# Kernel optimization log

Measured on AMD Instinct MI355X. Metric: run time of the kernel, lower is better.

The kernel has to match this reference:

```python
import jax, jax.numpy as jnp
import numpy as np

B, C, D = 4, 1024, 1024
H, DH = 16, 64  # num_heads, head_size; D == H*DH


def setup_inputs() -> dict:
    key = jax.random.key(0)
    ks = jax.random.split(key, 8)
    return {
        "query_input": jax.random.normal(ks[0], (B, C, D), dtype=jnp.float32),
        "key_input": jax.random.normal(ks[1], (B, C, D), dtype=jnp.float32),
        "value_input": jax.random.normal(ks[2], (B, C, D), dtype=jnp.float32),
        "Wq": jax.random.normal(ks[3], (D, D), dtype=jnp.float32) * 0.02,
        "Wk": jax.random.normal(ks[4], (D, D), dtype=jnp.float32) * 0.02,
        "Wv": jax.random.normal(ks[5], (D, D), dtype=jnp.float32) * 0.02,
        "Wp": jax.random.normal(ks[6], (D, D), dtype=jnp.float32) * 0.02,
        "bp": jax.random.normal(ks[7], (D,), dtype=jnp.float32) * 0.02,
        "mask": jnp.zeros((C, C), dtype=bool),
    }


def _split_heads(x):
    # (B, C, D) -> (B, H, C, DH)
    return x.reshape(B, C, H, DH).transpose(0, 2, 1, 3)


def reference(query_input, key_input, value_input, Wq, Wk, Wv, Wp, bp, mask):
    scale = DH ** -0.5
    q = _split_heads(query_input @ Wq.T)
    k = _split_heads(key_input @ Wk.T)
    v = _split_heads(value_input @ Wv.T)
    # ||q_i - k_j||_2 via norm decomposition: |q|^2 + |k|^2 - 2 q.k
    q2 = jnp.sum(q * q, axis=-1)  # (B, H, C)
    k2 = jnp.sum(k * k, axis=-1)  # (B, H, C)
    qk = jnp.einsum("bhqd,bhkd->bhqk", q, k)  # (B, H, C, C)
    sq = jnp.maximum(q2[..., :, None] + k2[..., None, :] - 2.0 * qk, 0.0)
    wei = jnp.sqrt(sq) * scale
    wei = jnp.where(mask, -jnp.inf, wei)
    wei = jax.nn.softmax(wei, axis=-1)
    out = jnp.einsum("bhqk,bhkd->bhqd", wei, v)  # (B, H, C, DH)
    out = out.transpose(0, 2, 1, 3).reshape(B, C, D)
    return out @ Wp.T + bp
```

## Files before the change

### kernel.cpp

```cpp
#include <hip/hip_runtime.h>


typedef _Float16 f16;
typedef __attribute__((ext_vector_type(2))) _Float16 f16x2;
typedef __attribute__((ext_vector_type(8))) _Float16 f16x8;
typedef __attribute__((ext_vector_type(4))) float f32x4;
typedef __attribute__((ext_vector_type(16))) float f32x16;

#define MFMA16(a, b, c) __builtin_amdgcn_mfma_f32_16x16x32_f16((a), (b), (c), 0, 0, 0)
#define MFMA32(a, b, c) __builtin_amdgcn_mfma_f32_32x32x16_f16((a), (b), (c), 0, 0, 0)

constexpr double LOG2E = 1.4426950408889634;
constexpr double C2d = 0.015625 * LOG2E * LOG2E;

#if __has_builtin(__builtin_amdgcn_exp2f)
#define EXP2F(x) __builtin_amdgcn_exp2f(x)
#else
#define EXP2F(x) exp2f(x)
#endif
#if __has_builtin(__builtin_amdgcn_sqrtf)
#define SQRTF(x) __builtin_amdgcn_sqrtf(x)
#else
#define SQRTF(x) sqrtf(x)
#endif

__device__ __forceinline__ void stage16(const void* g, void* lds_base_uniform) {
#if __has_builtin(__builtin_amdgcn_global_load_lds)
    __builtin_amdgcn_global_load_lds((const __attribute__((address_space(1))) void*)g,
                                     (__attribute__((address_space(3))) void*)lds_base_uniform,
                                     16, 0, 0);
#else
    const int lane = threadIdx.x & 63;
    *(f16x8*)((f16*)lds_base_uniform + lane * 8) = *(const f16x8*)g;
#endif
}

__device__ __forceinline__ f16x8 cvt8v(f32x4 a, f32x4 b) {
    f16x8 o;
    o[0] = (f16)a[0]; o[1] = (f16)a[1]; o[2] = (f16)a[2]; o[3] = (f16)a[3];
    o[4] = (f16)b[0]; o[5] = (f16)b[1]; o[6] = (f16)b[2]; o[7] = (f16)b[3];
    return o;
}

__global__ __launch_bounds__(256) void cvt_all(const float* __restrict__ Xq,
                                               const float* __restrict__ Xk,
                                               const float* __restrict__ Xv,
                                               const float* __restrict__ Wq,
                                               const float* __restrict__ Wk,
                                               const float* __restrict__ Wv,
                                               const float* __restrict__ Wp,
                                               f16* __restrict__ W16,
                                               f16* __restrict__ X16) {
    const size_t idx = (size_t)blockIdx.x * 2048 + threadIdx.x * 8;
    const size_t M4 = 4ull << 20, M1 = 1ull << 20;
    const float* s;
    f16* d;
    if (idx < 3 * M4) {
        if (idx < M4) s = Xq + idx;
        else if (idx < 2 * M4) s = Xk + (idx - M4);
        else s = Xv + (idx - 2 * M4);
        d = X16 + idx;
    } else {
        size_t wi = idx - 3 * M4;
        if (wi < M1) s = Wq + wi;
        else if (wi < 2 * M1) s = Wk + (wi - M1);
        else if (wi < 3 * M1) s = Wv + (wi - 2 * M1);
        else s = Wp + (wi - 3 * M1);
        d = W16 + wi;
    }
    f32x4 a = *(const f32x4*)s;
    f32x4 b = *(const f32x4*)(s + 4);
    *(f16x8*)d = cvt8v(a, b);
}

template <int MODE>
__global__ __launch_bounds__(256, 2) void gemm(const f16* __restrict__ A,
                                               const f16* __restrict__ B,
                                               f16* __restrict__ Co,
                                               float* __restrict__ Cf,
                                               const float* __restrict__ bias,
                                               float* __restrict__ nrm,
                                               float osc0, float osc1,
                                               float ns0, float ns1,
                                               int M, int N, int K) {
    constexpr bool NORMS = (MODE == 0);
    constexpr bool F32OUT = (MODE == 2);
    __shared__ __attribute__((aligned(16))) f16 As[128 * 64];
    __shared__ __attribute__((aligned(16))) f16 Bs[128 * 64];
    const int tid = threadIdx.x;
    const int lane = tid & 63;
    const int w = tid >> 6;
    const int l31 = lane & 31, l5 = lane >> 5;
    const int z = blockIdx.z;
    const f16* Ap = (MODE == 0) ? A + (size_t)z * (4u << 20) : A;
    const f16* Bp = (MODE == 0) ? B + (size_t)z * (1u << 20) : B;
    f16* Cop = (MODE == 0) ? Co + (size_t)z * (4u << 20) : Co;
    float* nrmp = NORMS ? nrm + (size_t)z * 65536 : nullptr;
    const float osc = z ? osc1 : osc0;
    const float nscale = z ? ns1 : ns0;
    const int wr = (w >> 1) * 64, wc = (w & 1) * 64;
    const int nwg = gridDim.x * gridDim.y;
    const int f = blockIdx.y * gridDim.x + blockIdx.x;
    const int g = (f & 7) * (nwg >> 3) + (f >> 3);
    const int row0 = (g / gridDim.x) * 128;
    const int col0 = (g % gridDim.x) * 128;

    f32x16 acc[2][2] = {};

    for (int kt = 0; kt < K; kt += 64) {
        __syncthreads();
#pragma unroll
        for (int t = 0; t < 4; ++t) {
            const int rb = w * 32 + t * 8;
            const int rr = rb + (lane >> 3);
            const int gs = (lane & 7) ^ (rr & 7);
            stage16(&Ap[(size_t)(row0 + rr) * K + kt + gs * 8], &As[rb * 64]);
            stage16(&Bp[(size_t)(col0 + rr) * K + kt + gs * 8], &Bs[rb * 64]);
        }
        __syncthreads();
#pragma unroll
        for (int ks = 0; ks < 4; ++ks) {
            const int gq = ks * 2 + l5;
            f16x8 af[2], bf[2];
#pragma unroll
            for (int mr = 0; mr < 2; ++mr)
                af[mr] = *(const f16x8*)&As[(wr + mr * 32 + l31) * 64 + ((gq ^ (l31 & 7)) * 8)];
#pragma unroll
            for (int n2 = 0; n2 < 2; ++n2)
                bf[n2] = *(const f16x8*)&Bs[(wc + n2 * 32 + l31) * 64 + ((gq ^ (l31 & 7)) * 8)];
#pragma unroll
            for (int mr = 0; mr < 2; ++mr)
#pragma unroll
                for (int n2 = 0; n2 < 2; ++n2) acc[mr][n2] = MFMA32(af[mr], bf[n2], acc[mr][n2]);
        }
    }

    const int cc0 = col0 + wc + l31;
    const int cc1 = col0 + wc + 32 + l31;
    const int hh = (col0 + wc) >> 6;
#pragma unroll
    for (int mr = 0; mr < 2; ++mr)
#pragma unroll
        for (int j = 0; j < 16; ++j) {
            const int rr = row0 + wr + mr * 32 + (j & 3) + 8 * (j >> 2) + 4 * l5;
            if (F32OUT) {
                Cf[(size_t)rr * N + cc0] = acc[mr][0][j] + bias[cc0];
                Cf[(size_t)rr * N + cc1] = acc[mr][1][j] + bias[cc1];
            } else {
                const f16 h0 = (f16)(acc[mr][0][j] * osc);
                const f16 h1 = (f16)(acc[mr][1][j] * osc);
                if (NORMS) {
                    float v0 = (float)h0, v1 = (float)h1;
                    float s = v0 * v0 + v1 * v1;
                    s += __shfl_xor(s, 1);
                    s += __shfl_xor(s, 2);
                    s += __shfl_xor(s, 4);
                    s += __shfl_xor(s, 8);
                    s += __shfl_xor(s, 16);
                    if (l31 == 0)
                        nrmp[(size_t)((rr >> 10) * 16 + hh) * 1024 + (rr & 1023)] = s * nscale;
                }
                Cop[(size_t)rr * N + cc0] = h0;
                Cop[(size_t)rr * N + cc1] = h1;
            }
        }
}

__global__ __launch_bounds__(256, 2) void attn(const f16* __restrict__ qs,
                                               const f16* __restrict__ kb,
                                               const f16* __restrict__ vT,
                                               const float* __restrict__ q2c2,
                                               const float* __restrict__ k2c2,
                                               f16* __restrict__ out) {
    __shared__ __attribute__((aligned(16))) f16 Ks[128 * 64];
    __shared__ __attribute__((aligned(16))) f16 Vs[64 * 128];
    __shared__ float k2tile[128];
    const int tid = threadIdx.x;
    const int lane = tid & 63;
    const int w = tid >> 6;
    const int l15 = lane & 15, l4 = lane >> 4;
    const int fid = blockIdx.y * 8 + blockIdx.x;
    const int qt = (fid >> 3) & 7;
    const int bh = (fid & 7) * 8 + (fid >> 6);
    const int b = bh >> 4, h = bh & 15;
    const int wq = w * 32;
    const int hcol = h * 64;
    const int qrow0 = b * 1024 + qt * 128;
    const f16* vTh = vT + (size_t)hcol * 4096 + b * 1024;

    const int sr = tid >> 3, sc0 = (tid & 7) * 8;
    const int vr = tid >> 4, vc0 = (tid & 15) * 8;
    const int vsw = (vr & 7) << 3;
    const int fsw = (l15 & 7) << 3;

    f16x8 bq[2][2];
#pragma unroll
    for (int m = 0; m < 2; ++m)
#pragma unroll
        for (int ks = 0; ks < 2; ++ks)
            bq[m][ks] = *(const f16x8*)&qs[(size_t)(qrow0 + wq + m * 16 + l15) * 1024 + hcol + ks * 32 + l4 * 8];
    float q2m[2];
#pragma unroll
    for (int m = 0; m < 2; ++m) q2m[m] = q2c2[(size_t)bh * 1024 + qt * 128 + wq + m * 16 + l15];

    f32x4 accv[2][4] = {};
    f32x4 dacc[2] = {};
    const f16 one = (f16)1.f;
    const f16x8 ones8 = {one, one, one, one, one, one, one, one};

    f16x8 kreg[4], vreg[4];
    float k2reg = 0.f;
#define ISSUE_LOADS(KT)                                                                                      \
    {                                                                                                        \
        _Pragma("unroll") for (int i = 0; i < 4; ++i)                                                        \
            kreg[i] = *(const f16x8*)&kb[(size_t)(b * 1024 + (KT) * 128 + sr + i * 32) * 1024 + hcol + sc0]; \
        _Pragma("unroll") for (int j = 0; j < 4; ++j)                                                        \
            vreg[j] = *(const f16x8*)&vTh[(size_t)(vr + j * 16) * 4096 + (KT) * 128 + vc0];                  \
        k2reg = (tid < 128) ? k2c2[(size_t)bh * 1024 + (KT) * 128 + tid] : 0.f;                              \
    }

    ISSUE_LOADS(0)

    for (int kt = 0; kt < 8; ++kt) {
        __syncthreads();
#pragma unroll
        for (int i = 0; i < 4; ++i) {
            const int kap = sr + i * 32;
            const int s = ((kap >> 5) & 3) * 32 + ((kap >> 2) & 1) * 16 + ((kap >> 3) & 3) * 4 + (kap & 3);
            *(f16x8*)&Ks[s * 64 + (sc0 ^ ((s & 7) << 3))] = kreg[i];
        }
#pragma unroll
        for (int j = 0; j < 4; ++j) *(f16x8*)&Vs[(vr + j * 16) * 128 + (vc0 ^ vsw)] = vreg[j];
        if (tid < 128) k2tile[tid] = k2reg;
        __syncthreads();
        if (kt < 7) ISSUE_LOADS(kt + 1)

#pragma unroll
        for (int kk = 0; kk < 4; ++kk) {
            unsigned um[2][4];
#pragma unroll
            for (int half = 0; half < 2; ++half) {
                const int n = kk * 2 + half;
                f16x8 kf0 = *(const f16x8*)&Ks[(n * 16 + l15) * 64 + ((l4 * 8) ^ fsw)];
                f16x8 kf1 = *(const f16x8*)&Ks[(n * 16 + l15) * 64 + ((32 + l4 * 8) ^ fsw)];
                f32x4 k2q = *(const f32x4*)&k2tile[kk * 32 + l4 * 8 + half * 4];
#pragma unroll
                for (int m = 0; m < 2; ++m) {
                    f32x4 c0;
#pragma unroll
                    for (int r = 0; r < 4; ++r) c0[r] = q2m[m] + k2q[r];
                    f32x4 st = MFMA16(kf0, bq[m][0], c0);
                    st = MFMA16(kf1, bq[m][1], st);
                    float p0 = EXP2F(SQRTF(fmaxf(st[0], 0.f)));
                    float p1 = EXP2F(SQRTF(fmaxf(st[1], 0.f)));
                    float p2 = EXP2F(SQRTF(fmaxf(st[2], 0.f)));
                    float p3 = EXP2F(SQRTF(fmaxf(st[3], 0.f)));
                    f16x2 lo = {(f16)p0, (f16)p1};
                    f16x2 hi = {(f16)p2, (f16)p3};
                    um[m][half * 2] = __builtin_bit_cast(unsigned, lo);
                    um[m][half * 2 + 1] = __builtin_bit_cast(unsigned, hi);
                }
            }
            f16x8 ap[2];
#pragma unroll
            for (int m = 0; m < 2; ++m) {
                uint4 u = {um[m][0], um[m][1], um[m][2], um[m][3]};
                ap[m] = __builtin_bit_cast(f16x8, u);
            }
#pragma unroll
            for (int m = 0; m < 2; ++m) dacc[m] = MFMA16(ap[m], ones8, dacc[m]);
#pragma unroll
            for (int n2 = 0; n2 < 4; ++n2) {
                f16x8 bv = *(const f16x8*)&Vs[(n2 * 16 + l15) * 128 + ((kk * 32 + l4 * 8) ^ fsw)];
#pragma unroll
                for (int m = 0; m < 2; ++m) accv[m][n2] = MFMA16(ap[m], bv, accv[m][n2]);
            }
        }
    }

#pragma unroll
    for (int m = 0; m < 2; ++m)
#pragma unroll
        for (int r = 0; r < 4; ++r) {
            const float rd = 1.0f / dacc[m][r];
#pragma unroll
            for (int n2 = 0; n2 < 4; ++n2)
                out[(size_t)(qrow0 + wq + m * 16 + l4 * 4 + r) * 1024 + hcol + n2 * 16 + l15] =
                    (f16)(accv[m][n2][r] * rd);
        }
}

extern "C" void kernel_launch(void* const* d_in, const int* in_sizes, int n_in,
                              void* d_out, int out_size, void* d_ws, size_t ws_size,
                              hipStream_t stream) {
    const float* Xq = (const float*)d_in[0];
    const float* Xk = (const float*)d_in[1];
    const float* Xv = (const float*)d_in[2];
    const float* Wq = (const float*)d_in[3];
    const float* Wk = (const float*)d_in[4];
    const float* Wv = (const float*)d_in[5];
    const float* Wp = (const float*)d_in[6];
    const float* bp = (const float*)d_in[7];
    float* out = (float*)d_out;

    char* ws = (char*)d_ws;
    f16* W16 = (f16*)(ws);
    f16* X16 = (f16*)(ws + (8ull << 20));
    f16* vTb = (f16*)(ws + (8ull << 20));
    f16* attnout = (f16*)(ws + (16ull << 20));
    f16* Xv16 = (f16*)(ws + (24ull << 20));
    f16* qb = (f16*)(ws + (32ull << 20));
    f16* kb = (f16*)(ws + (40ull << 20));
    float* q2c2 = out;
    float* k2c2 = out + 65536;

    const float qsc = (float)(-2.0 * C2d);
    const float ns_q = (float)(1.0 / (4.0 * C2d));
    const float ns_k = (float)C2d;

    cvt_all<<<8192, 256, 0, stream>>>(Xq, Xk, Xv, Wq, Wk, Wv, Wp, W16, X16);

    gemm<0><<<dim3(8, 32, 2), 256, 0, stream>>>(
        X16, W16, qb, nullptr, nullptr, q2c2, qsc, 1.0f, ns_q, ns_k, 4096, 1024, 1024);

    gemm<1><<<dim3(32, 8), 256, 0, stream>>>(
        W16 + 2 * (1u << 20), Xv16, vTb, nullptr, nullptr, nullptr,
        1.0f, 1.0f, 0.f, 0.f, 1024, 4096, 1024);

    attn<<<dim3(8, 64), 256, 0, stream>>>(qb, kb, vTb, q2c2, k2c2, attnout);

    gemm<2><<<dim3(8, 32), 256, 0, stream>>>(
        attnout, W16 + 3 * (1u << 20), nullptr, out, bp, nullptr,
        1.0f, 1.0f, 0.f, 0.f, 4096, 1024, 1024);
}
```

Measured before the change: 119.3 us.

## Split attention KV loop across two thread groups and merge QKV gemm launches

The attention kernel now runs 512 threads per block. Two groups of 256 each process half of the key tiles, and their partial accumulators are reduced through shared memory before normalisation. The Q/K and V projection gemms are merged into one launch, and the output projection uses 64x128 tiles to double the block count. MFMA sections get raised wave priority. The aim is more parallelism and fewer launches, at the cost of higher LDS use per block and an extra reduction step.

```diff
diff --git a/kernel.cpp b/kernel.cpp
--- a/kernel.cpp
+++ b/kernel.cpp
@@ -73,37 +73,21 @@
     *(f16x8*)d = cvt8v(a, b);
 }
 
-template <int MODE>
-__global__ __launch_bounds__(256, 2) void gemm(const f16* __restrict__ A,
-                                               const f16* __restrict__ B,
-                                               f16* __restrict__ Co,
-                                               float* __restrict__ Cf,
-                                               const float* __restrict__ bias,
-                                               float* __restrict__ nrm,
-                                               float osc0, float osc1,
-                                               float ns0, float ns1,
-                                               int M, int N, int K) {
-    constexpr bool NORMS = (MODE == 0);
-    constexpr bool F32OUT = (MODE == 2);
-    __shared__ __attribute__((aligned(16))) f16 As[128 * 64];
-    __shared__ __attribute__((aligned(16))) f16 Bs[128 * 64];
+template <bool NORMS, bool F32OUT>
+__device__ __forceinline__ void gemm128(f16* As, f16* Bs,
+                                        const f16* __restrict__ Ap,
+                                        const f16* __restrict__ Bp,
+                                        f16* __restrict__ Cop,
+                                        float* __restrict__ Cf,
+                                        const float* __restrict__ bias,
+                                        float* __restrict__ nrmp,
+                                        float osc, float nscale,
+                                        int row0, int col0, int N, int K) {
     const int tid = threadIdx.x;
     const int lane = tid & 63;
     const int w = tid >> 6;
     const int l31 = lane & 31, l5 = lane >> 5;
-    const int z = blockIdx.z;
-    const f16* Ap = (MODE == 0) ? A + (size_t)z * (4u << 20) : A;
-    const f16* Bp = (MODE == 0) ? B + (size_t)z * (1u << 20) : B;
-    f16* Cop = (MODE == 0) ? Co + (size_t)z * (4u << 20) : Co;
-    float* nrmp = NORMS ? nrm + (size_t)z * 65536 : nullptr;
-    const float osc = z ? osc1 : osc0;
-    const float nscale = z ? ns1 : ns0;
     const int wr = (w >> 1) * 64, wc = (w & 1) * 64;
-    const int nwg = gridDim.x * gridDim.y;
-    const int f = blockIdx.y * gridDim.x + blockIdx.x;
-    const int g = (f & 7) * (nwg >> 3) + (f >> 3);
-    const int row0 = (g / gridDim.x) * 128;
-    const int col0 = (g % gridDim.x) * 128;
 
     f32x16 acc[2][2] = {};
 
@@ -166,30 +150,126 @@
         }
 }
 
-__global__ __launch_bounds__(256, 2) void attn(const f16* __restrict__ qs,
+__global__ __launch_bounds__(256, 2) void gemm_qkv(const f16* __restrict__ X16,
+                                                   const f16* __restrict__ W16,
+                                                   f16* __restrict__ qb_base,
+                                                   f16* __restrict__ vTb,
+                                                   float* __restrict__ nrm,
+                                                   float qsc, float ns_q, float ns_k) {
+    __shared__ __attribute__((aligned(16))) f16 As[128 * 64];
+    __shared__ __attribute__((aligned(16))) f16 Bs[128 * 64];
+    const int bid = blockIdx.x;
+    if (bid < 512) {
+        const int z = bid >> 8;
+        const int f = bid & 255;
+        const int g = (f & 7) * 32 + (f >> 3);
+        const int row0 = (g >> 3) * 128, col0 = (g & 7) * 128;
+        gemm128<true, false>(As, Bs,
+                             X16 + (size_t)z * (4u << 20), W16 + (size_t)z * (1u << 20),
+                             qb_base + (size_t)z * (4u << 20), nullptr, nullptr,
+                             nrm + (size_t)z * 65536,
+                             z ? 1.0f : qsc, z ? ns_k : ns_q, row0, col0, 1024, 1024);
+    } else {
+        const int f = bid - 512;
+        const int g = (f & 7) * 32 + (f >> 3);
+        const int row0 = (g >> 5) * 128, col0 = (g & 31) * 128;
+        gemm128<false, false>(As, Bs,
+                              W16 + 2 * (1u << 20), X16 + 2 * (4u << 20),
+                              vTb, nullptr, nullptr, nullptr,
+                              1.0f, 0.f, row0, col0, 4096, 1024);
+    }
+}
+
+__global__ __launch_bounds__(256, 2) void gemm_fin(const f16* __restrict__ A,
+                                                   const f16* __restrict__ B,
+                                                   float* __restrict__ Cf,
+                                                   const float* __restrict__ bias) {
+    __shared__ __attribute__((aligned(16))) f16 As[64 * 64];
+    __shared__ __attribute__((aligned(16))) f16 Bs[128 * 64];
+    const int tid = threadIdx.x;
+    const int lane = tid & 63;
+    const int w = tid >> 6;
+    const int l31 = lane & 31, l5 = lane >> 5;
+    const int wr = (w & 1) * 32, wc = (w >> 1) * 64;
+    const int f = blockIdx.x;
+    const int g = (f & 7) * 64 + (f >> 3);
+    const int row0 = (g >> 3) * 64, col0 = (g & 7) * 128;
+    const int K = 1024, N = 1024;
+
+    f32x16 acc[2] = {};
+
+    for (int kt = 0; kt < K; kt += 64) {
+        __syncthreads();
+#pragma unroll
+        for (int t = 0; t < 2; ++t) {
+            const int rb = w * 16 + t * 8;
+            const int rr = rb + (lane >> 3);
+            const int gs = (lane & 7) ^ (rr & 7);
+            stage16(&A[(size_t)(row0 + rr) * K + kt + gs * 8], &As[rb * 64]);
+        }
+#pragma unroll
+        for (int t = 0; t < 4; ++t) {
+            const int rb = w * 32 + t * 8;
+            const int rr = rb + (lane >> 3);
+            const int gs = (lane & 7) ^ (rr & 7);
+            stage16(&B[(size_t)(col0 + rr) * K + kt + gs * 8], &Bs[rb * 64]);
+        }
+        __syncthreads();
+#pragma unroll
+        for (int ks = 0; ks < 4; ++ks) {
+            const int gq = ks * 2 + l5;
+            f16x8 af = *(const f16x8*)&As[(wr + l31) * 64 + ((gq ^ (l31 & 7)) * 8)];
+#pragma unroll
+            for (int n2 = 0; n2 < 2; ++n2) {
+                f16x8 bf = *(const f16x8*)&Bs[(wc + n2 * 32 + l31) * 64 + ((gq ^ (l31 & 7)) * 8)];
+                acc[n2] = MFMA32(af, bf, acc[n2]);
+            }
+        }
+    }
+
+    const int cc0 = col0 + wc + l31;
+    const int cc1 = col0 + wc + 32 + l31;
+#pragma unroll
+    for (int j = 0; j < 16; ++j) {
+        const int rr = row0 + wr + (j & 3) + 8 * (j >> 2) + 4 * l5;
+        Cf[(size_t)rr * N + cc0] = acc[0][j] + bias[cc0];
+        Cf[(size_t)rr * N + cc1] = acc[1][j] + bias[cc1];
+    }
+}
+
+__global__ __launch_bounds__(512, 4) void attn(const f16* __restrict__ qs,
                                                const f16* __restrict__ kb,
                                                const f16* __restrict__ vT,
                                                const float* __restrict__ q2c2,
                                                const float* __restrict__ k2c2,
                                                f16* __restrict__ out) {
-    __shared__ __attribute__((aligned(16))) f16 Ks[128 * 64];
-    __shared__ __attribute__((aligned(16))) f16 Vs[64 * 128];
-    __shared__ float k2tile[128];
+    __shared__ __attribute__((aligned(16))) char smem[67 * 1024];
+    f16* KsA = (f16*)smem;
+    f16* VsA = (f16*)(smem + 32768);
+    float* k2tA = (float*)(smem + 65536);
+    float* mbuf = (float*)smem;
+
     const int tid = threadIdx.x;
+    const int grp = tid >> 8;
+    const int t2 = tid & 255;
     const int lane = tid & 63;
-    const int w = tid >> 6;
+    const int w4 = t2 >> 6;
     const int l15 = lane & 15, l4 = lane >> 4;
+    f16* Ks = KsA + grp * (128 * 64);
+    f16* Vs = VsA + grp * (64 * 128);
+    float* k2t = k2tA + grp * 128;
+
     const int fid = blockIdx.y * 8 + blockIdx.x;
     const int qt = (fid >> 3) & 7;
     const int bh = (fid & 7) * 8 + (fid >> 6);
     const int b = bh >> 4, h = bh & 15;
-    const int wq = w * 32;
+    const int wq = w4 * 32;
     const int hcol = h * 64;
     const int qrow0 = b * 1024 + qt * 128;
     const f16* vTh = vT + (size_t)hcol * 4096 + b * 1024;
 
-    const int sr = tid >> 3, sc0 = (tid & 7) * 8;
-    const int vr = tid >> 4, vc0 = (tid & 15) * 8;
+    const int sr = t2 >> 3, sc0 = (t2 & 7) * 8;
+    const int vr = t2 >> 4, vc0 = (t2 & 15) * 8;
     const int vsw = (vr & 7) << 3;
     const int fsw = (l15 & 7) << 3;
 
@@ -216,12 +296,12 @@
             kreg[i] = *(const f16x8*)&kb[(size_t)(b * 1024 + (KT) * 128 + sr + i * 32) * 1024 + hcol + sc0]; \
         _Pragma("unroll") for (int j = 0; j < 4; ++j)                                                        \
             vreg[j] = *(const f16x8*)&vTh[(size_t)(vr + j * 16) * 4096 + (KT) * 128 + vc0];                  \
-        k2reg = (tid < 128) ? k2c2[(size_t)bh * 1024 + (KT) * 128 + tid] : 0.f;                              \
-    }
-
-    ISSUE_LOADS(0)
-
-    for (int kt = 0; kt < 8; ++kt) {
+        k2reg = (t2 < 128) ? k2c2[(size_t)bh * 1024 + (KT) * 128 + t2] : 0.f;                                \
+    }
+
+    ISSUE_LOADS(grp * 4)
+
+    for (int ktl = 0; ktl < 4; ++ktl) {
         __syncthreads();
 #pragma unroll
         for (int i = 0; i < 4; ++i) {
@@ -231,9 +311,9 @@
         }
 #pragma unroll
         for (int j = 0; j < 4; ++j) *(f16x8*)&Vs[(vr + j * 16) * 128 + (vc0 ^ vsw)] = vreg[j];
-        if (tid < 128) k2tile[tid] = k2reg;
-        __syncthreads();
-        if (kt < 7) ISSUE_LOADS(kt + 1)
+        if (t2 < 128) k2t[t2] = k2reg;
+        __syncthreads();
+        if (ktl < 3) ISSUE_LOADS(grp * 4 + ktl + 1)
 
 #pragma unroll
         for (int kk = 0; kk < 4; ++kk) {
@@ -243,7 +323,7 @@
                 const int n = kk * 2 + half;
                 f16x8 kf0 = *(const f16x8*)&Ks[(n * 16 + l15) * 64 + ((l4 * 8) ^ fsw)];
                 f16x8 kf1 = *(const f16x8*)&Ks[(n * 16 + l15) * 64 + ((32 + l4 * 8) ^ fsw)];
-                f32x4 k2q = *(const f32x4*)&k2tile[kk * 32 + l4 * 8 + half * 4];
+                f32x4 k2q = *(const f32x4*)&k2t[kk * 32 + l4 * 8 + half * 4];
 #pragma unroll
                 for (int m = 0; m < 2; ++m) {
                     f32x4 c0;
@@ -267,6 +347,7 @@
                 uint4 u = {um[m][0], um[m][1], um[m][2], um[m][3]};
                 ap[m] = __builtin_bit_cast(f16x8, u);
             }
+            __builtin_amdgcn_s_setprio(1);
 #pragma unroll
             for (int m = 0; m < 2; ++m) dacc[m] = MFMA16(ap[m], ones8, dacc[m]);
 #pragma unroll
@@ -275,19 +356,40 @@
 #pragma unroll
                 for (int m = 0; m < 2; ++m) accv[m][n2] = MFMA16(ap[m], bv, accv[m][n2]);
             }
-        }
-    }
-
-#pragma unroll
-    for (int m = 0; m < 2; ++m)
-#pragma unroll
-        for (int r = 0; r < 4; ++r) {
-            const float rd = 1.0f / dacc[m][r];
-#pragma unroll
-            for (int n2 = 0; n2 < 4; ++n2)
-                out[(size_t)(qrow0 + wq + m * 16 + l4 * 4 + r) * 1024 + hcol + n2 * 16 + l15] =
-                    (f16)(accv[m][n2][r] * rd);
-        }
+            __builtin_amdgcn_s_setprio(0);
+        }
+    }
+
+    __syncthreads();
+    if (grp) {
+        float* p = mbuf + t2 * 40;
+#pragma unroll
+        for (int m = 0; m < 2; ++m)
+#pragma unroll
+            for (int n2 = 0; n2 < 4; ++n2) *(f32x4*)(p + (m * 4 + n2) * 4) = accv[m][n2];
+        *(f32x4*)(p + 32) = dacc[0];
+        *(f32x4*)(p + 36) = dacc[1];
+    }
+    __syncthreads();
+    if (!grp) {
+        float* p = mbuf + t2 * 40;
+#pragma unroll
+        for (int m = 0; m < 2; ++m)
+#pragma unroll
+            for (int n2 = 0; n2 < 4; ++n2) accv[m][n2] += *(const f32x4*)(p + (m * 4 + n2) * 4);
+        dacc[0] += *(const f32x4*)(p + 32);
+        dacc[1] += *(const f32x4*)(p + 36);
+#pragma unroll
+        for (int m = 0; m < 2; ++m)
+#pragma unroll
+            for (int r = 0; r < 4; ++r) {
+                const float rd = 1.0f / dacc[m][r];
+#pragma unroll
+                for (int n2 = 0; n2 < 4; ++n2)
+                    out[(size_t)(qrow0 + wq + m * 16 + l4 * 4 + r) * 1024 + hcol + n2 * 16 + l15] =
+                        (f16)(accv[m][n2][r] * rd);
+            }
+    }
 }
 
 extern "C" void kernel_launch(void* const* d_in, const int* in_sizes, int n_in,
@@ -306,11 +408,11 @@
     char* ws = (char*)d_ws;
     f16* W16 = (f16*)(ws);
     f16* X16 = (f16*)(ws + (8ull << 20));
-    f16* vTb = (f16*)(ws + (8ull << 20));
-    f16* attnout = (f16*)(ws + (16ull << 20));
-    f16* Xv16 = (f16*)(ws + (24ull << 20));
     f16* qb = (f16*)(ws + (32ull << 20));
     f16* kb = (f16*)(ws + (40ull << 20));
+    f16* vTb = (f16*)(ws + (48ull << 20));
+    f16* attnout = (f16*)(ws + (56ull << 20));
+    (void)kb;
     float* q2c2 = out;
     float* k2c2 = out + 65536;
 
@@ -320,16 +422,9 @@
 
     cvt_all<<<8192, 256, 0, stream>>>(Xq, Xk, Xv, Wq, Wk, Wv, Wp, W16, X16);
 
-    gemm<0><<<dim3(8, 32, 2), 256, 0, stream>>>(
-        X16, W16, qb, nullptr, nullptr, q2c2, qsc, 1.0f, ns_q, ns_k, 4096, 1024, 1024);
-
-    gemm<1><<<dim3(32, 8), 256, 0, stream>>>(
-        W16 + 2 * (1u << 20), Xv16, vTb, nullptr, nullptr, nullptr,
-        1.0f, 1.0f, 0.f, 0.f, 1024, 4096, 1024);
-
-    attn<<<dim3(8, 64), 256, 0, stream>>>(qb, kb, vTb, q2c2, k2c2, attnout);
-
-    gemm<2><<<dim3(8, 32), 256, 0, stream>>>(
-        attnout, W16 + 3 * (1u << 20), nullptr, out, bp, nullptr,
-        1.0f, 1.0f, 0.f, 0.f, 4096, 1024, 1024);
-}
+    gemm_qkv<<<768, 256, 0, stream>>>(X16, W16, qb, vTb, q2c2, qsc, ns_q, ns_k);
+
+    attn<<<dim3(8, 64), 512, 0, stream>>>(qb, kb, vTb, q2c2, k2c2, attnout);
+
+    gemm_fin<<<512, 256, 0, stream>>>(attnout, W16 + 3 * (1u << 20), out, bp);
+}
```

Measured after the change: 113.3 us. 5.1% less time.
